# Kernel optimization log

Hardware: AMD Instinct MI355X
Metric: run time of the kernel (lower is better)

Reference implementation:

```python
import jax, jax.numpy as jnp
import numpy as np

PART = 0  # index of '<PART>' tag in vocab (select_part_tag = zeros)
W = 3     # max_word_len


def lstm_scan(x_seq, h0, c0, Wih, Whh, bih, bhh):
    """x_seq: [S, N, D] -> outputs [S, N, H]. torch LSTM gate order i, f, g, o."""
    def cell(carry, x):
        h, c = carry
        g = x @ Wih.T + bih + h @ Whh.T + bhh
        i, f, gg, o = jnp.split(g, 4, axis=-1)
        c = jax.nn.sigmoid(f) * c + jax.nn.sigmoid(i) * jnp.tanh(gg)
        h = jax.nn.sigmoid(o) * jnp.tanh(c)
        return (h, c), h
    _, hs = jax.lax.scan(cell, (h0, c0), x_seq)
    return hs


def decoder_probs(win, h0, emb, Wih, Whh, bih, bhh, Wp, bp):
    """Decoder.forward for all start positions at once.
    win: [N, W] candidate-word tokens; h0: [N, H] (used as both h0 and c0).
    Returns [W, N]: row y = log p(word win[:, :y+1] then <PART>)."""
    N = win.shape[0]
    toks = jnp.concatenate([jnp.full((N, 1), PART, win.dtype), win], axis=1)  # prepend <PART>
    x = jnp.swapaxes(emb[toks], 0, 1)                    # [W+1, N, D]
    hs = lstm_scan(x, h0, h0, Wih, Whh, bih, bhh)        # [W+1, N, H]
    logits = hs @ Wp.T + bp                              # [W+1, N, V]
    logZ = jax.nn.logsumexp(logits, axis=-1)             # [W+1, N]
    # log_softmax gathered at target char / <PART> tag positions
    char = jnp.take_along_axis(logits[:-1], win.T[:, :, None], axis=-1)[..., 0] - logZ[:-1]  # [W, N]
    tag = logits[1:, :, PART] - logZ[1:]                 # [W, N]
    return jnp.cumsum(char, axis=0) + tag                # cumulative char logprob + end tag


def forward_loss(sentence, emb, enc, decf, decb):
    B, T = sentence.shape
    H = enc[1].shape[1]
    fvec = sentence
    bvec = jnp.flip(sentence, axis=1)

    def encode(vec):
        toks = jnp.concatenate([jnp.full((B, 1), PART, vec.dtype), vec[:, :-1]], axis=1)
        x = jnp.swapaxes(emb[toks], 0, 1)                # [T, B, D]
        z = jnp.zeros((B, H), emb.dtype)
        return lstm_scan(x, z, z, *enc)                  # [T, B, H]

    enc_f, enc_b = encode(fvec), encode(bvec)
    idx = jnp.clip(jnp.arange(T)[:, None] + jnp.arange(W)[None, :], 0, T - 1)  # [T, W]

    def run_dec(vec, enc_out, params):
        win = vec[:, idx].reshape(B * T, W)              # window starting at each position
        h0 = jnp.swapaxes(enc_out, 0, 1).reshape(B * T, -1)
        p = decoder_probs(win, h0, emb, *params)         # [W, B*T]
        return p.reshape(W, B, T).transpose(2, 0, 1)     # [T(start), W(len-1), B]

    fwdP = run_dec(fvec, enc_f, decf)
    bwdP = run_dec(bvec, enc_b, decb)

    xs = jnp.arange(T)[:, None]
    ys = jnp.arange(W)[None, :]
    # SGB_A.add_bidirection: P[x, y, b] = score of word of length y+1 ending at position x
    P = 0.5 * (fwdP[jnp.clip(xs - ys, 0, T - 1), ys] + bwdP[T - 1 - xs, ys])  # [T, W, B]

    # compute_all_probability: semi-CRF forward recursion
    NEG = jnp.asarray(-1e30, P.dtype)
    def step(buf, inp):
        # buf[i] = total[j-1-i]
        p_j, j = inp
        cand = jnp.where((jnp.arange(W) < j)[:, None], buf + p_j, NEG)
        tot = jax.nn.logsumexp(cand, axis=0)
        return jnp.concatenate([tot[None], buf[:-1]], axis=0), tot

    _, totals = jax.lax.scan(step, jnp.zeros((W, B), P.dtype), (P, jnp.arange(1, T + 1)))
    return -jnp.mean(totals[-1])


def setup_inputs() -> dict:
    key = jax.random.key(0)
    V, D, H, B, T = 8000, 256, 256, 16, 128
    ks = jax.random.split(key, 24)
    s_d = 1.0 / np.sqrt(D)
    s_h = 1.0 / np.sqrt(H)

    def mat(k, shape, scale):
        return jax.random.normal(k, shape, jnp.float32) * scale

    def lstm_p(k):
        k1, k2, k3, k4 = jax.random.split(k, 4)
        return (mat(k1, (4 * H, D), s_d), mat(k2, (4 * H, H), s_h),
                mat(k3, (4 * H,), s_h), mat(k4, (4 * H,), s_h))

    enc = lstm_p(ks[1])
    decf_l = lstm_p(ks[2])
    decb_l = lstm_p(ks[3])
    inp = {
        "sentence": jax.random.randint(ks[0], (B, T), 0, V, jnp.int32),
        "emb": mat(ks[4], (V, D), 1.0),
        "enc_Wih": enc[0], "enc_Whh": enc[1], "enc_bih": enc[2], "enc_bhh": enc[3],
        "decf_Wih": decf_l[0], "decf_Whh": decf_l[1], "decf_bih": decf_l[2], "decf_bhh": decf_l[3],
        "decf_Wp": mat(ks[5], (V, H), s_h), "decf_bp": mat(ks[6], (V,), s_h),
        "decb_Wih": decb_l[0], "decb_Whh": decb_l[1], "decb_bih": decb_l[2], "decb_bhh": decb_l[3],
        "decb_Wp": mat(ks[7], (V, H), s_h), "decb_bp": mat(ks[8], (V,), s_h),
    }
    return inp


def reference(sentence, emb, enc_Wih, enc_Whh, enc_bih, enc_bhh,
              decf_Wih, decf_Whh, decf_bih, decf_bhh, decf_Wp, decf_bp,
              decb_Wih, decb_Whh, decb_bih, decb_bhh, decb_Wp, decb_bp):
    return forward_loss(
        sentence, emb,
        (enc_Wih, enc_Whh, enc_bih, enc_bhh),
        (decf_Wih, decf_Whh, decf_bih, decf_bhh, decf_Wp, decf_bp),
        (decb_Wih, decb_Whh, decb_bih, decb_bhh, decb_Wp, decb_bp))
```

## Files before the change

kernel.cpp:

```cpp
#include <hip/hip_runtime.h>
#include <math.h>

#define VOCAB 8000
#define NN 2048

typedef unsigned short u16;
typedef __attribute__((ext_vector_type(8))) short short8v;
typedef __attribute__((ext_vector_type(4))) short short4v;
typedef __attribute__((ext_vector_type(4))) float float4v;
typedef __attribute__((ext_vector_type(4))) int int4v;

#define OFF_WPBF   0ul
#define OFF_WDEC   2048000ul
#define OFF_XENC   2572288ul
#define OFF_H0BF   4153344ul
#define OFF_DECX   4677632ul
#define OFF_CDEC   6250496ul
#define OFF_HSBF   7299072ul
#define OFF_GBUF   9396224ul
#define OFF_LOGZ   13590528ul
#define OFF_GCH    13606912ul
#define OFF_GTG    13619200ul
#define OFF_P      13631488ul
#define OFF_WTOK   13637632ul
#define OFF_XP0    13649920ul
#define OFF_ENCW   13652032ul
#define OFF_SENC   13914240ul
#define OFF_SQ     13915264ul
#define OFF_WQI8   13916288ul
#define OFF_GXD    13981824ul
#define WS_NEED_OV ((OFF_GXD + 6291456ul) * 4ul)

__device__ __forceinline__ float sigf(float x) { return 1.0f / (1.0f + __expf(-x)); }
__device__ __forceinline__ float tanhsafe(float x) {
    x = fminf(15.0f, fmaxf(-15.0f, x));
    float e = __expf(2.0f * x);
    return (e - 1.0f) / (e + 1.0f);
}
__device__ __forceinline__ u16 f2bf(float f) {
    union { float f; unsigned int u; } x; x.f = f;
    return (u16)((x.u + 0x7fffu + ((x.u >> 16) & 1u)) >> 16);
}
__device__ __forceinline__ float bf2f(u16 x) {
    union { unsigned int u; float f; } v; v.u = ((unsigned int)x) << 16;
    return v.f;
}

__device__ __forceinline__ short8v ldfrag(const u16* lds, int row, int k, int lane, int SB) {
    int r = row + (lane & 15);
    int off = r * SB + ((k + ((lane >> 4) << 3)) << 1);
    off ^= (r & 7) << 4;
    return *(const short8v*)((const char*)lds + off);
}

__device__ __forceinline__ void stage128x256(const u16* __restrict__ g, int row0, int rowmax,
                                             int rowstride, int col0, u16* lds, int tid) {
    #pragma unroll
    for (int it = 0; it < 16; ++it) {
        int chunk = tid + it * 256;
        int r = chunk >> 5;
        int kc = (chunk & 31) << 3;
        short8v v = {0, 0, 0, 0, 0, 0, 0, 0};
        if (row0 + r < rowmax)
            v = *(const short8v*)(g + (size_t)(row0 + r) * rowstride + col0 + kc);
        int off = (r * 512 + kc * 2) ^ ((r & 7) << 4);
        *(short8v*)((char*)lds + off) = v;
    }
}

__global__ __launch_bounds__(256) void k_setup(const int* __restrict__ S,
                                               const float* __restrict__ emb,
                                               const float* __restrict__ eWih, const float* __restrict__ eWhh,
                                               const float* __restrict__ fWih, const float* __restrict__ fWhh,
                                               const float* __restrict__ fWp,
                                               const float* __restrict__ bWih, const float* __restrict__ bWhh,
                                               const float* __restrict__ bWp,
                                               u16* __restrict__ WpBF, u16* __restrict__ WdecBF,
                                               u16* __restrict__ encW,
                                               float* __restrict__ s_enc, signed char* __restrict__ wq,
                                               u16* __restrict__ xEncBF,
                                               u16* __restrict__ decX, int* __restrict__ winTok,
                                               float* __restrict__ xp0) {
    const int b = blockIdx.x, tid = threadIdx.x;
    if (b < 2000) {
        int chunk = b * 256 + tid;
        int kc = (chunk & 31) << 3;
        int v = (chunk >> 5) % 8000;
        int d = chunk / (8000 * 32);
        const float* src = (d ? bWp : fWp) + (size_t)v * 256 + kc;
        u16 t8[8];
        #pragma unroll
        for (int j = 0; j < 8; ++j) t8[j] = f2bf(src[j]);
        *(short8v*)(WpBF + ((size_t)d * 8000 + v) * 256 + kc) = *(short8v*)t8;
    } else if (b < 2512) {
        int chunk = (b - 2000) * 256 + tid;
        int kc = (chunk & 63) << 3;
        int r = (chunk >> 6) & 1023;
        int d = chunk >> 16;
        const float* Whh = d ? bWhh : fWhh;
        const float* Wih = d ? bWih : fWih;
        const float* src = (kc < 256) ? (Whh + (size_t)r * 256 + kc) : (Wih + (size_t)r * 256 + (kc - 256));
        u16 t8[8];
        #pragma unroll
        for (int j = 0; j < 8; ++j) t8[j] = f2bf(src[j]);
        *(short8v*)(WdecBF + ((size_t)d * 1024 + r) * 512 + kc) = *(short8v*)t8;
    } else if (b < 2768) {
        int chunk = (b - 2512) * 256 + tid;
        int kc = (chunk & 63) << 3;
        int r = chunk >> 6;
        const float* src = (kc < 256) ? (eWhh + (size_t)r * 256 + kc) : (eWih + (size_t)r * 256 + (kc - 256));
        u16 t8[8];
        #pragma unroll
        for (int j = 0; j < 8; ++j) t8[j] = f2bf(src[j]);
        *(short8v*)(encW + (size_t)r * 512 + kc) = *(short8v*)t8;
    } else if (b < 2832) {
        int lin = (b - 2768) * 256 + tid;
        int lane = lin & 63;
        int ks = (lin >> 6) & 3;
        int c = (lin >> 8) & 3;
        int w = lin >> 10;
        int r = c * 256 + w * 16 + (lane & 15);
        float m = 0.0f;
        for (int k = 0; k < 256; k += 4) {
            float4 v4 = *(const float4*)(eWhh + (size_t)r * 256 + k);
            m = fmaxf(m, fmaxf(fmaxf(fabsf(v4.x), fabsf(v4.y)), fmaxf(fabsf(v4.z), fabsf(v4.w))));
        }
        float sqv = (m > 0.0f) ? 127.0f / m : 0.0f;
        if (ks == 0 && lane < 16) s_enc[r] = m / 16129.0f;
        int kb = ks * 64 + ((lane >> 4) << 4);
        signed char o16[16];
        #pragma unroll
        for (int j = 0; j < 16; ++j) {
            float q = rintf(eWhh[(size_t)r * 256 + kb + j] * sqv);
            q = fminf(127.0f, fmaxf(-127.0f, q));
            o16[j] = (signed char)q;
        }
        *(int4v*)(wq + (size_t)lin * 16) = *(int4v*)o16;
    } else if (b < 3344) {
        int chunk = (b - 2832) * 256 + tid;
        int kc = (chunk & 31) << 3;
        int bb = (chunk >> 5) & 15;
        int t = (chunk >> 9) & 127;
        int d = chunk >> 16;
        int tok = 0;
        if (t > 0) tok = d ? S[bb * 128 + 128 - t] : S[bb * 128 + t - 1];
        const float* src = emb + (size_t)tok * 256 + kc;
        u16 t8[8];
        #pragma unroll
        for (int j = 0; j < 8; ++j) t8[j] = f2bf(src[j]);
        *(short8v*)(xEncBF + (size_t)(((d * 128 + t) * 16) + bb) * 256 + kc) = *(short8v*)t8;
    } else if (b < 4880) {
        int chunk = (b - 3344) * 256 + tid;
        int kc = (chunk & 31) << 3;
        int n = (chunk >> 5) & 2047;
        int r2 = chunk >> 16;
        int s = r2 % 3, d = r2 / 3;
        int bb = n >> 7, tq = n & 127;
        int pos = min(tq + s, 127);
        int tok = d ? S[bb * 128 + 127 - pos] : S[bb * 128 + pos];
        const float* src = emb + (size_t)tok * 256 + kc;
        u16 t8[8];
        #pragma unroll
        for (int j = 0; j < 8; ++j) t8[j] = f2bf(src[j]);
        *(short8v*)(decX + ((size_t)(d * 3 + s) * NN + n) * 256 + kc) = *(short8v*)t8;
        if ((chunk & 31) == 0) winTok[(d * 3 + s) * NN + n] = tok;
    } else {
        int idx = (b - 4880) * 256 + tid;
        int d = idx >> 10, r = idx & 1023;
        const float* Wih = d ? bWih : fWih;
        float acc = 0.0f;
        for (int k = 0; k < 256; ++k) acc = fmaf(emb[k], Wih[r * 256 + k], acc);
        xp0[idx] = acc;
    }
}

__global__ __launch_bounds__(256) void k_xproj(const u16* __restrict__ xEncBF,
                                               const u16* __restrict__ encW,
                                               const float* __restrict__ ebih,
                                               const float* __restrict__ ebhh,
                                               float* __restrict__ xpT) {
    __shared__ u16 At[128 * 256];
    __shared__ u16 Bt[128 * 256];
    const int tid = threadIdx.x, lane = tid & 63, wid = tid >> 6;
    const int wm = wid >> 1, wv = wid & 1;
    const int r0 = blockIdx.x * 128, n0 = blockIdx.y * 128, d = blockIdx.z;
    stage128x256(xEncBF + (size_t)d * 2048 * 256, n0, 1 << 30, 256, 0, At, tid);
    stage128x256(encW, r0, 1 << 30, 512, 256, Bt, tid);
    __syncthreads();
    float4v acc[4][4];
    #pragma unroll
    for (int m = 0; m < 4; ++m)
        #pragma unroll
        for (int v = 0; v < 4; ++v) acc[m][v] = (float4v){0.f, 0.f, 0.f, 0.f};
    #pragma unroll
    for (int k = 0; k < 8; ++k) {
        short8v af[4], bf[4];
        #pragma unroll
        for (int m = 0; m < 4; ++m) af[m] = ldfrag(At, wm * 64 + m * 16, k * 32, lane, 512);
        #pragma unroll
        for (int v = 0; v < 4; ++v) bf[v] = ldfrag(Bt, wv * 64 + v * 16, k * 32, lane, 512);
        #pragma unroll
        for (int m = 0; m < 4; ++m)
            #pragma unroll
            for (int v = 0; v < 4; ++v)
                acc[m][v] = __builtin_amdgcn_mfma_f32_16x16x32_bf16(af[m], bf[v], acc[m][v], 0, 0, 0);
    }
    float bs[4]; int rg[4];
    #pragma unroll
    for (int v = 0; v < 4; ++v) {
        rg[v] = r0 + wv * 64 + v * 16 + (lane & 15);
        bs[v] = ebih[rg[v]] + ebhh[rg[v]];
    }
    #pragma unroll
    for (int m = 0; m < 4; ++m)
        #pragma unroll
        for (int i = 0; i < 4; ++i) {
            int n = n0 + wm * 64 + m * 16 + ((lane >> 4) << 2) + i;
            int t_ = n >> 4, bfull = n & 15;
            #pragma unroll
            for (int v = 0; v < 4; ++v) {
                int g = rg[v] >> 8, u = rg[v] & 255;
                size_t idx4 = (((size_t)(d * 16 + bfull) * 128 + t_) * 16 + (u >> 4)) * 16 + (u & 15);
                xpT[idx4 * 4 + g] = acc[m][v][i] + bs[v];
            }
        }
}

__global__ __launch_bounds__(1024) void k_encx(const signed char* __restrict__ wq,
                                               const float* __restrict__ s_enc,
                                               const float4v* __restrict__ xpT4,
                                               u16* __restrict__ h0bf,
                                               const u16* __restrict__ decXBF,
                                               const u16* __restrict__ WdecBF,
                                               const float* __restrict__ fbih, const float* __restrict__ fbhh,
                                               const float* __restrict__ bbih, const float* __restrict__ bbhh,
                                               u16* __restrict__ gXdec) {
    __shared__ char smem[131072];
    const int tid = threadIdx.x, lane = tid & 63, w = tid >> 6;
    const int l15 = lane & 15, hi = lane >> 4;
    if (blockIdx.x < 32) {
        signed char (*hbuf)[4096] = (signed char(*)[4096])smem;
        const int blk = blockIdx.x, d = blk >> 4, b = blk & 15;
        int4v breg[4][4];
        #pragma unroll
        for (int c = 0; c < 4; ++c)
            #pragma unroll
            for (int ks = 0; ks < 4; ++ks)
                breg[c][ks] = *(const int4v*)(wq + ((size_t)(((w * 4 + c) * 4 + ks) * 64 + lane)) * 16);
        float sreg[4];
        #pragma unroll
        for (int c = 0; c < 4; ++c) sreg[c] = s_enc[c * 256 + w * 16 + l15];
        float creg = 0.0f;
        ((long*)hbuf)[tid & 1023] = 0l;
        const bool cellane = (lane < 16);
        const int u = w * 16 + l15;
        const float4v* xbase = xpT4 + ((size_t)(d * 16 + b) * 128) * 256 + w * 16 + l15;
        float4v xv_next = {0.f, 0.f, 0.f, 0.f};
        if (cellane) xv_next = xbase[0];
        __syncthreads();
        for (int t = 0; t < 128; ++t) {
            int cur = t & 1;
            float4v xv = xv_next;
            if (cellane && t < 127) xv_next = xbase[(size_t)(t + 1) * 256];
            int4v af[4];
            #pragma unroll
            for (int ks = 0; ks < 4; ++ks) {
                int off = (l15 * 256 + ks * 64 + hi * 16) ^ ((l15 & 7) << 4);
                af[ks] = *(const int4v*)(hbuf[cur] + off);
            }
            int4v acc[4];
            #pragma unroll
            for (int c = 0; c < 4; ++c) {
                acc[c] = (int4v){0, 0, 0, 0};
                #pragma unroll
                for (int ks = 0; ks < 4; ++ks)
                    acc[c] = __builtin_amdgcn_mfma_i32_16x16x64_i8(af[ks], breg[c][ks], acc[c], 0, 0, 0);
            }
            if (cellane) {
                float gi = (float)acc[0][0] * sreg[0] + xv[0];
                float gf = (float)acc[1][0] * sreg[1] + xv[1];
                float gG = (float)acc[2][0] * sreg[2] + xv[2];
                float go = (float)acc[3][0] * sreg[3] + xv[3];
                float cn = sigf(gf) * creg + sigf(gi) * tanhsafe(gG);
                float h = sigf(go) * tanhsafe(cn);
                creg = cn;
                h0bf[((size_t)d * NN + b * 128 + t) * 256 + u] = f2bf(h);
                hbuf[cur ^ 1][u] = (signed char)rintf(h * 127.0f);
            }
            __syncthreads();
        }
    } else {
        u16* At = (u16*)smem;
        u16* Bt = (u16*)(smem + 65536);
        const int bi = blockIdx.x - 32;
        const int rt = bi & 7, nt = (bi >> 3) & 15, rest = bi >> 7;
        const int sx = rest % 3, d = rest / 3;
        const int r0 = rt * 128, n0 = nt * 128;
        const int wm = w >> 2, wv = w & 3;
        const u16* Asrc = decXBF + (size_t)(d * 3 + sx) * NN * 256;
        const u16* Bsrc = WdecBF + (size_t)d * 1024 * 512;
        #pragma unroll
        for (int it = 0; it < 4; ++it) {
            int chunk = tid + it * 1024;
            int r = chunk >> 5, kc = (chunk & 31) << 3;
            short8v va = *(const short8v*)(Asrc + (size_t)(n0 + r) * 256 + kc);
            short8v vb = *(const short8v*)(Bsrc + (size_t)(r0 + r) * 512 + 256 + kc);
            int off = (r * 512 + kc * 2) ^ ((r & 7) << 4);
            *(short8v*)((char*)At + off) = va;
            *(short8v*)((char*)Bt + off) = vb;
        }
        __syncthreads();
        float4v acc[2][2];
        #pragma unroll
        for (int m = 0; m < 2; ++m)
            #pragma unroll
            for (int v = 0; v < 2; ++v) acc[m][v] = (float4v){0.f, 0.f, 0.f, 0.f};
        #pragma unroll
        for (int kk = 0; kk < 8; ++kk) {
            short8v af[2], bf[2];
            #pragma unroll
            for (int m = 0; m < 2; ++m) af[m] = ldfrag(At, wm * 32 + m * 16, kk * 32, lane, 512);
            #pragma unroll
            for (int v = 0; v < 2; ++v) bf[v] = ldfrag(Bt, wv * 32 + v * 16, kk * 32, lane, 512);
            #pragma unroll
            for (int m = 0; m < 2; ++m)
                #pragma unroll
                for (int v = 0; v < 2; ++v)
                    acc[m][v] = __builtin_amdgcn_mfma_f32_16x16x32_bf16(af[m], bf[v], acc[m][v], 0, 0, 0);
        }
        const float* bih = d ? bbih : fbih;
        const float* bhh = d ? bbhh : fbhh;
        #pragma unroll
        for (int m = 0; m < 2; ++m)
            #pragma unroll
            for (int i = 0; i < 4; ++i) {
                int n = n0 + wm * 32 + m * 16 + hi * 4 + i;
                #pragma unroll
                for (int v = 0; v < 2; ++v) {
                    int r = r0 + wv * 32 + v * 16 + l15;
                    float val = acc[m][v][i] + bih[r] + bhh[r];
                    gXdec[((size_t)(d * 3 + sx) * NN + n) * 1024 + r] = f2bf(val);
                }
            }
    }
}

__global__ __launch_bounds__(256) void k_decmm(const u16* __restrict__ Ah, size_t ahStride,
                                               const u16* __restrict__ Axx, size_t axStride,
                                               const u16* __restrict__ Wdec,
                                               const float* __restrict__ bihf, const float* __restrict__ bhhf,
                                               const float* __restrict__ bihb, const float* __restrict__ bhhb,
                                               const float* __restrict__ xp0, int s,
                                               const u16* __restrict__ gXdec,
                                               float* __restrict__ gBuf) {
    __shared__ u16 At[128 * 256];
    __shared__ u16 Bt[128 * 256];
    const int tid = threadIdx.x, lane = tid & 63, wid = tid >> 6;
    const int wm = wid >> 1, wv = wid & 1;
    const int r0 = blockIdx.x * 128, n0 = blockIdx.y * 128, d = blockIdx.z;
    float4v acc[4][4];
    #pragma unroll
    for (int m = 0; m < 4; ++m)
        #pragma unroll
        for (int v = 0; v < 4; ++v) acc[m][v] = (float4v){0.f, 0.f, 0.f, 0.f};
    const int useX = (s >= 1);
    const int nph = (useX && !gXdec) ? 2 : 1;
    for (int ph = 0; ph < nph; ++ph) {
        const u16* Asrc = (ph == 0) ? (Ah + (size_t)d * ahStride) : (Axx + (size_t)d * axStride);
        stage128x256(Asrc, n0, 1 << 30, 256, 0, At, tid);
        stage128x256(Wdec + (size_t)d * 1024 * 512, r0, 1 << 30, 512, ph * 256, Bt, tid);
        __syncthreads();
        #pragma unroll
        for (int k = 0; k < 8; ++k) {
            short8v af[4], bf[4];
            #pragma unroll
            for (int m = 0; m < 4; ++m) af[m] = ldfrag(At, wm * 64 + m * 16, k * 32, lane, 512);
            #pragma unroll
            for (int v = 0; v < 4; ++v) bf[v] = ldfrag(Bt, wv * 64 + v * 16, k * 32, lane, 512);
            #pragma unroll
            for (int m = 0; m < 4; ++m)
                #pragma unroll
                for (int v = 0; v < 4; ++v)
                    acc[m][v] = __builtin_amdgcn_mfma_f32_16x16x32_bf16(af[m], bf[v], acc[m][v], 0, 0, 0);
        }
        __syncthreads();
    }
    const float* bih = d ? bihb : bihf;
    const float* bhh = d ? bhhb : bhhf;
    int rg[4];
    float bs[4] = {0.f, 0.f, 0.f, 0.f};
    #pragma unroll
    for (int v = 0; v < 4; ++v) {
        rg[v] = r0 + wv * 64 + v * 16 + (lane & 15);
        if (!useX) bs[v] = bih[rg[v]] + bhh[rg[v]] + xp0[d * 1024 + rg[v]];
        else if (!gXdec) bs[v] = bih[rg[v]] + bhh[rg[v]];
    }
    #pragma unroll
    for (int m = 0; m < 4; ++m)
        #pragma unroll
        for (int i = 0; i < 4; ++i) {
            int n = n0 + wm * 64 + m * 16 + ((lane >> 4) << 2) + i;
            #pragma unroll
            for (int v = 0; v < 4; ++v) {
                float g = acc[m][v][i] + bs[v];
                if (useX && gXdec)
                    g += bf2f(gXdec[((size_t)(d * 3 + s - 1) * NN + n) * 1024 + rg[v]]);
                gBuf[((size_t)d * NN + n) * 1024 + rg[v]] = g;
            }
        }
}

__global__ __launch_bounds__(256) void k_deccell(const float* __restrict__ gBuf,
                                                 const u16* __restrict__ h0bf,
                                                 float* __restrict__ cDec,
                                                 u16* __restrict__ hsBF, int s) {
    int flat = blockIdx.x * 256 + threadIdx.x;
    int j = flat & 255;
    int n = (flat >> 8) & 2047;
    int d = flat >> 19;
    const float* g = gBuf + ((size_t)d * NN + n) * 1024;
    float gi = g[j], gf = g[j + 256], gg = g[j + 512], go = g[j + 768];
    float cprev = (s == 0) ? bf2f(h0bf[flat]) : cDec[flat];
    float cn = sigf(gf) * cprev + sigf(gi) * tanhsafe(gg);
    float h = sigf(go) * tanhsafe(cn);
    cDec[flat] = cn;
    hsBF[((size_t)(d * 4 + s) * NN + n) * 256 + j] = f2bf(h);
}

__global__ __launch_bounds__(512, 2) void k_proj8(const u16* __restrict__ hsBF,
                                                  const u16* __restrict__ WpBF,
                                                  const float* __restrict__ bpf, const float* __restrict__ bpb,
                                                  const int* __restrict__ winTok,
                                                  float* __restrict__ partials,
                                                  float* __restrict__ gchar, float* __restrict__ gtag) {
    __shared__ u16 At[128 * 256];
    __shared__ u16 Bt[2][64 * 256];
    const int tid = threadIdx.x, lane = tid & 63, w = tid >> 6;
    const int wm = w >> 1, wv = w & 1;
    const int l15 = lane & 15, hi = lane >> 4;
    const int L = blockIdx.x;
    const int chunkI = L & 7, idx = L >> 3;
    const int n0 = (idx & 15) * 128, d = idx >> 4;
    const int vt0 = chunkI * 16;
    const int nvt = min(16, 125 - vt0);
    const float* bp = d ? bpb : bpf;

#define LOADB8(vt_) do {                                                          \
        _Pragma("unroll")                                                         \
        for (int it = 0; it < 4; ++it) {                                          \
            int g = tid + it * 512; int r = g >> 5, kc = (g & 31) << 3;           \
            bregs[it] = *(const short8v*)(WpBF + ((size_t)d * 8000 + (vt_) * 64 + r) * 256 + kc); \
        }                                                                         \
    } while (0)
#define WRITEB8(buf_) do {                                                        \
        _Pragma("unroll")                                                         \
        for (int it = 0; it < 4; ++it) {                                          \
            int g = tid + it * 512; int r = g >> 5, kc = (g & 31) << 3;           \
            int off = (r * 512 + kc * 2) ^ ((r & 7) << 4);                        \
            *(short8v*)((char*)Bt[buf_] + off) = bregs[it];                       \
        }                                                                         \
    } while (0)

    short8v bregs[4];
    for (int s = 0; s < 4; ++s) {
        const u16* hsA = hsBF + (size_t)(d * 4 + s) * NN * 256;
        #pragma unroll
        for (int it = 0; it < 8; ++it) {
            int chunk = tid + it * 512;
            int r = chunk >> 5, kc = (chunk & 31) << 3;
            short8v v8 = *(const short8v*)(hsA + (size_t)(n0 + r) * 256 + kc);
            int off = (r * 512 + kc * 2) ^ ((r & 7) << 4);
            *(short8v*)((char*)At + off) = v8;
        }
        LOADB8(vt0);
        WRITEB8(0);
        int tok[2][4];
        #pragma unroll
        for (int m = 0; m < 2; ++m)
            #pragma unroll
            for (int i = 0; i < 4; ++i) {
                int n = n0 + wm * 32 + m * 16 + hi * 4 + i;
                tok[m][i] = (s < 3) ? winTok[(d * 3 + s) * NN + n] : -1;
            }
        float expsum[2][4] = {{0.f, 0.f, 0.f, 0.f}, {0.f, 0.f, 0.f, 0.f}};
        __syncthreads();
        short8v afr[2][8];
        #pragma unroll
        for (int m = 0; m < 2; ++m)
            #pragma unroll
            for (int kk = 0; kk < 8; ++kk) {
                afr[m][kk] = ldfrag(At, wm * 32 + m * 16, kk * 32, lane, 512);
                asm volatile("" : "+v"(afr[m][kk]));
            }
        int cur = 0;
        for (int t = 0; t < nvt; ++t) {
            int vt = vt0 + t;
            if (t + 1 < nvt) LOADB8(vt + 1);
            float bpv[2];
            #pragma unroll
            for (int v = 0; v < 2; ++v) bpv[v] = bp[vt * 64 + wv * 32 + v * 16 + l15];
            float4v acc[2][2];
            #pragma unroll
            for (int m = 0; m < 2; ++m)
                #pragma unroll
                for (int v = 0; v < 2; ++v) acc[m][v] = (float4v){0.f, 0.f, 0.f, 0.f};
            #pragma unroll
            for (int kk = 0; kk < 8; ++kk) {
                short8v bf[2];
                #pragma unroll
                for (int v = 0; v < 2; ++v) bf[v] = ldfrag(Bt[cur], wv * 32 + v * 16, kk * 32, lane, 512);
                #pragma unroll
                for (int m = 0; m < 2; ++m)
                    #pragma unroll
                    for (int v = 0; v < 2; ++v)
                        acc[m][v] = __builtin_amdgcn_mfma_f32_16x16x32_bf16(afr[m][kk], bf[v], acc[m][v], 0, 0, 0);
            }
            #pragma unroll
            for (int m = 0; m < 2; ++m)
                #pragma unroll
                for (int i = 0; i < 4; ++i) {
                    int n = n0 + wm * 32 + m * 16 + hi * 4 + i;
                    float es = 0.0f;
                    #pragma unroll
                    for (int v = 0; v < 2; ++v) {
                        int vgv = vt * 64 + wv * 32 + v * 16 + l15;
                        float lg = acc[m][v][i] + bpv[v];
                        es += __expf(lg);
                        if (vgv == tok[m][i]) gchar[(d * 3 + s) * NN + n] = lg;
                        if (s >= 1 && vgv == 0) gtag[(d * 3 + (s - 1)) * NN + n] = lg;
                    }
                    expsum[m][i] += es;
                }
            __syncthreads();
            if (t + 1 < nvt) WRITEB8(cur ^ 1);
            __syncthreads();
            cur ^= 1;
        }
        #pragma unroll
        for (int m = 0; m < 2; ++m)
            #pragma unroll
            for (int i = 0; i < 4; ++i) {
                float e = expsum[m][i];
                #pragma unroll
                for (int off = 1; off <= 8; off <<= 1) e += __shfl_xor(e, off);
                if (l15 == 0) {
                    int n = n0 + wm * 32 + m * 16 + hi * 4 + i;
                    partials[((size_t)(d * 4 + s) * NN + n) * 16 + chunkI * 2 + wv] = e;
                }
            }
    }
#undef LOADB8
#undef WRITEB8
}

__global__ __launch_bounds__(256) void k_lzsum(const float* __restrict__ partials,
                                               float* __restrict__ logZ) {
    int row = blockIdx.x * 256 + threadIdx.x;
    const float* p = partials + (size_t)row * 16;
    float s = 0.0f;
    #pragma unroll
    for (int c = 0; c < 16; ++c) s += p[c];
    logZ[row] = __logf(s);
}

__global__ __launch_bounds__(256) void k_passm(const float* __restrict__ gchar,
                                               const float* __restrict__ gtag,
                                               const float* __restrict__ logZ,
                                               float* __restrict__ P) {
    int flat = blockIdx.x * 256 + threadIdx.x;
    if (flat >= 128 * 3 * 16) return;
    int b = flat & 15;
    int y = (flat >> 4) % 3;
    int x = flat / 48;
    int nf = b * 128 + min(127, max(0, x - y));
    int nb = b * 128 + 127 - x;
    float pf = 0.0f, pb = 0.0f;
    for (int ss = 0; ss <= y; ++ss) {
        pf += gchar[ss * NN + nf] - logZ[ss * NN + nf];
        pb += gchar[(3 + ss) * NN + nb] - logZ[(4 + ss) * NN + nb];
    }
    pf += gtag[y * NN + nf] - logZ[(y + 1) * NN + nf];
    pb += gtag[(3 + y) * NN + nb] - logZ[(4 + y + 1) * NN + nb];
    P[flat] = 0.5f * (pf + pb);
}

__global__ __launch_bounds__(64) void k_scan(const float* __restrict__ P, float* __restrict__ out) {
    __shared__ float Pl[128 * 48];
    int tid = threadIdx.x;
    #pragma unroll
    for (int it = 0; it < 96; ++it) Pl[tid + it * 64] = P[tid + it * 64];
    __syncthreads();
    if (tid < 16) {
        int b = tid;
        float b0 = 0.f, b1 = 0.f, b2 = 0.f, tot = 0.f;
        for (int j = 1; j <= 128; ++j) {
            float c0 = b0 + Pl[((j - 1) * 3 + 0) * 16 + b];
            float c1 = (j >= 2) ? b1 + Pl[((j - 1) * 3 + 1) * 16 + b] : -1e30f;
            float c2 = (j >= 3) ? b2 + Pl[((j - 1) * 3 + 2) * 16 + b] : -1e30f;
            float mx = fmaxf(c0, fmaxf(c1, c2));
            float sv = __expf(c0 - mx) + __expf(c1 - mx) + __expf(c2 - mx);
            tot = mx + __logf(sv);
            b2 = b1; b1 = b0; b0 = tot;
        }
        #pragma unroll
        for (int off = 1; off <= 8; off <<= 1) tot += __shfl_xor(tot, off);
        if (b == 0) out[0] = -tot / 16.0f;
    }
}

extern "C" void kernel_launch(void* const* d_in, const int* in_sizes, int n_in,
                              void* d_out, int out_size, void* d_ws, size_t ws_size,
                              hipStream_t stream) {
    const int* S = (const int*)d_in[0];
    const float* emb = (const float*)d_in[1];
    const float* eWih = (const float*)d_in[2];
    const float* eWhh = (const float*)d_in[3];
    const float* ebih = (const float*)d_in[4];
    const float* ebhh = (const float*)d_in[5];
    const float* fWih = (const float*)d_in[6];
    const float* fWhh = (const float*)d_in[7];
    const float* fbih = (const float*)d_in[8];
    const float* fbhh = (const float*)d_in[9];
    const float* fWp  = (const float*)d_in[10];
    const float* fbp  = (const float*)d_in[11];
    const float* bWih = (const float*)d_in[12];
    const float* bWhh = (const float*)d_in[13];
    const float* bbih = (const float*)d_in[14];
    const float* bbhh = (const float*)d_in[15];
    const float* bWp  = (const float*)d_in[16];
    const float* bbp  = (const float*)d_in[17];

    float* w = (float*)d_ws;
    u16* WpBF    = (u16*)(w + OFF_WPBF);
    u16* WdecBF  = (u16*)(w + OFF_WDEC);
    u16* xEncBF  = (u16*)(w + OFF_XENC);
    u16* h0bf    = (u16*)(w + OFF_H0BF);
    u16* decXBF  = (u16*)(w + OFF_DECX);
    float* cDec  = w + OFF_CDEC;
    u16* hsBF    = (u16*)(w + OFF_HSBF);
    float* gBuf  = w + OFF_GBUF;
    float* xpT   = gBuf;
    float* partials = gBuf;
    float* logZ  = w + OFF_LOGZ;
    float* gchar = w + OFF_GCH;
    float* gtag  = w + OFF_GTG;
    float* Pm    = w + OFF_P;
    int* winTok  = (int*)(w + OFF_WTOK);
    float* xp0   = w + OFF_XP0;
    u16* encW    = (u16*)(w + OFF_ENCW);
    float* sEnc  = w + OFF_SENC;
    signed char* wqEnc = (signed char*)(w + OFF_WQI8);
    u16* gXdec   = (u16*)(w + OFF_GXD);

    const bool useOv = (ws_size >= WS_NEED_OV);

    k_setup<<<4888, 256, 0, stream>>>(S, emb, eWih, eWhh, fWih, fWhh, fWp,
                                      bWih, bWhh, bWp,
                                      WpBF, WdecBF, encW, sEnc, wqEnc,
                                      xEncBF, decXBF, winTok, xp0);

    k_xproj<<<dim3(8, 16, 2), 256, 0, stream>>>(xEncBF, encW, ebih, ebhh, xpT);

    k_encx<<<useOv ? 800 : 32, 1024, 0, stream>>>(wqEnc, sEnc, (const float4v*)xpT, h0bf,
                                                  decXBF, WdecBF, fbih, fbhh, bbih, bbhh,
                                                  gXdec);

    const u16* gx = useOv ? gXdec : nullptr;
    for (int s = 0; s < 4; ++s) {
        const u16* Ah; size_t ahS;
        const u16* Axx; size_t axS;
        if (s == 0) {
            Ah = h0bf; ahS = (size_t)NN * 256;
            Axx = decXBF; axS = (size_t)3 * NN * 256;
        } else {
            Ah = hsBF + (size_t)(s - 1) * NN * 256; ahS = (size_t)4 * NN * 256;
            Axx = decXBF + (size_t)(s - 1) * NN * 256; axS = (size_t)3 * NN * 256;
        }
        k_decmm<<<dim3(8, 16, 2), 256, 0, stream>>>(Ah, ahS, Axx, axS, WdecBF,
                                                    fbih, fbhh, bbih, bbhh, xp0,
                                                    s, gx, gBuf);
        k_deccell<<<4096, 256, 0, stream>>>(gBuf, h0bf, cDec, hsBF, s);
    }

    k_proj8<<<256, 512, 0, stream>>>(hsBF, WpBF, fbp, bbp, winTok,
                                     partials, gchar, gtag);
    k_lzsum<<<64, 256, 0, stream>>>(partials, logZ);
    k_passm<<<24, 256, 0, stream>>>(gchar, gtag, logZ, Pm);
    k_scan<<<1, 64, 0, stream>>>(Pm, (float*)d_out);
}
```

Baseline: 473.3 us.

## Fuse decoder gate GEMM with LSTM cell and buffer encoder outputs in LDS

The decoder step's gate matmul and its LSTM cell update now run in one kernel. Each block stages the 32 hidden units' i/f/g/o weight rows, so all four gates for a unit sit in one tile. Gates go to shared memory and the cell runs in place, which drops the fp32 gBuf round trip through global memory and one launch per step. In the encoder, per-step h stores to global are replaced by an LDS history buffer copied out once at the end, and the x prefetch becomes a plain per-step load. The cost is 128KB of LDS per decoder block, which limits occupancy, and exposed x-load latency in the encoder.

```diff
diff --git a/kernel.cpp b/kernel.cpp
--- a/kernel.cpp
+++ b/kernel.cpp
@@ -240,6 +240,7 @@
     const int l15 = lane & 15, hi = lane >> 4;
     if (blockIdx.x < 32) {
         signed char (*hbuf)[4096] = (signed char(*)[4096])smem;
+        u16* hist = (u16*)(smem + 8192);
         const int blk = blockIdx.x, d = blk >> 4, b = blk & 15;
         int4v breg[4][4];
         #pragma unroll
@@ -255,13 +256,11 @@
         const bool cellane = (lane < 16);
         const int u = w * 16 + l15;
         const float4v* xbase = xpT4 + ((size_t)(d * 16 + b) * 128) * 256 + w * 16 + l15;
-        float4v xv_next = {0.f, 0.f, 0.f, 0.f};
-        if (cellane) xv_next = xbase[0];
         __syncthreads();
         for (int t = 0; t < 128; ++t) {
             int cur = t & 1;
-            float4v xv = xv_next;
-            if (cellane && t < 127) xv_next = xbase[(size_t)(t + 1) * 256];
+            float4v xv = {0.f, 0.f, 0.f, 0.f};
+            if (cellane) xv = xbase[(size_t)t * 256];
             int4v af[4];
             #pragma unroll
             for (int ks = 0; ks < 4; ++ks) {
@@ -284,11 +283,15 @@
                 float cn = sigf(gf) * creg + sigf(gi) * tanhsafe(gG);
                 float h = sigf(go) * tanhsafe(cn);
                 creg = cn;
-                h0bf[((size_t)d * NN + b * 128 + t) * 256 + u] = f2bf(h);
+                hist[t * 256 + u] = f2bf(h);
                 hbuf[cur ^ 1][u] = (signed char)rintf(h * 127.0f);
             }
             __syncthreads();
         }
+        long* dst = (long*)(h0bf + (size_t)(d * NN + b * 128) * 256);
+        const long* src = (const long*)hist;
+        #pragma unroll
+        for (int it = 0; it < 8; ++it) dst[tid + it * 1024] = src[tid + it * 1024];
     } else {
         u16* At = (u16*)smem;
         u16* Bt = (u16*)(smem + 65536);
@@ -345,19 +348,23 @@
     }
 }
 
-__global__ __launch_bounds__(256) void k_decmm(const u16* __restrict__ Ah, size_t ahStride,
-                                               const u16* __restrict__ Axx, size_t axStride,
-                                               const u16* __restrict__ Wdec,
-                                               const float* __restrict__ bihf, const float* __restrict__ bhhf,
-                                               const float* __restrict__ bihb, const float* __restrict__ bhhb,
-                                               const float* __restrict__ xp0, int s,
-                                               const u16* __restrict__ gXdec,
-                                               float* __restrict__ gBuf) {
-    __shared__ u16 At[128 * 256];
-    __shared__ u16 Bt[128 * 256];
+__global__ __launch_bounds__(256) void k_decf(const u16* __restrict__ Ah, size_t ahStride,
+                                              const u16* __restrict__ Axx, size_t axStride,
+                                              const u16* __restrict__ Wdec,
+                                              const float* __restrict__ bihf, const float* __restrict__ bhhf,
+                                              const float* __restrict__ bihb, const float* __restrict__ bhhb,
+                                              const float* __restrict__ xp0, int s,
+                                              const u16* __restrict__ gXdec,
+                                              const u16* __restrict__ h0bf,
+                                              float* __restrict__ cDec, u16* __restrict__ hsBF) {
+    __shared__ char smem[131072];
+    u16* At = (u16*)smem;
+    u16* Bt = (u16*)(smem + 65536);
+    float* gl = (float*)smem;
     const int tid = threadIdx.x, lane = tid & 63, wid = tid >> 6;
     const int wm = wid >> 1, wv = wid & 1;
-    const int r0 = blockIdx.x * 128, n0 = blockIdx.y * 128, d = blockIdx.z;
+    const int l15 = lane & 15, hi = lane >> 4;
+    const int u0 = blockIdx.x * 32, n0 = blockIdx.y * 128, d = blockIdx.z;
     float4v acc[4][4];
     #pragma unroll
     for (int m = 0; m < 4; ++m)
@@ -368,7 +375,15 @@
     for (int ph = 0; ph < nph; ++ph) {
         const u16* Asrc = (ph == 0) ? (Ah + (size_t)d * ahStride) : (Axx + (size_t)d * axStride);
         stage128x256(Asrc, n0, 1 << 30, 256, 0, At, tid);
-        stage128x256(Wdec + (size_t)d * 1024 * 512, r0, 1 << 30, 512, ph * 256, Bt, tid);
+        #pragma unroll
+        for (int it = 0; it < 16; ++it) {
+            int chunk = tid + it * 256;
+            int rl = chunk >> 5, kc = (chunk & 31) << 3;
+            int rglob = ((rl >> 5) << 8) + u0 + (rl & 31);
+            short8v v8 = *(const short8v*)(Wdec + ((size_t)d * 1024 + rglob) * 512 + ph * 256 + kc);
+            int off = (rl * 512 + kc * 2) ^ ((rl & 7) << 4);
+            *(short8v*)((char*)Bt + off) = v8;
+        }
         __syncthreads();
         #pragma unroll
         for (int k = 0; k < 8; ++k) {
@@ -387,44 +402,39 @@
     }
     const float* bih = d ? bihb : bihf;
     const float* bhh = d ? bhhb : bhhf;
-    int rg[4];
-    float bs[4] = {0.f, 0.f, 0.f, 0.f};
-    #pragma unroll
-    for (int v = 0; v < 4; ++v) {
-        rg[v] = r0 + wv * 64 + v * 16 + (lane & 15);
-        if (!useX) bs[v] = bih[rg[v]] + bhh[rg[v]] + xp0[d * 1024 + rg[v]];
-        else if (!gXdec) bs[v] = bih[rg[v]] + bhh[rg[v]];
-    }
     #pragma unroll
     for (int m = 0; m < 4; ++m)
         #pragma unroll
         for (int i = 0; i < 4; ++i) {
-            int n = n0 + wm * 64 + m * 16 + ((lane >> 4) << 2) + i;
+            int nl = wm * 64 + m * 16 + hi * 4 + i;
             #pragma unroll
             for (int v = 0; v < 4; ++v) {
-                float g = acc[m][v][i] + bs[v];
-                if (useX && gXdec)
-                    g += bf2f(gXdec[((size_t)(d * 3 + s - 1) * NN + n) * 1024 + rg[v]]);
-                gBuf[((size_t)d * NN + n) * 1024 + rg[v]] = g;
-            }
-        }
-}
-
-__global__ __launch_bounds__(256) void k_deccell(const float* __restrict__ gBuf,
-                                                 const u16* __restrict__ h0bf,
-                                                 float* __restrict__ cDec,
-                                                 u16* __restrict__ hsBF, int s) {
-    int flat = blockIdx.x * 256 + threadIdx.x;
-    int j = flat & 255;
-    int n = (flat >> 8) & 2047;
-    int d = flat >> 19;
-    const float* g = gBuf + ((size_t)d * NN + n) * 1024;
-    float gi = g[j], gf = g[j + 256], gg = g[j + 512], go = g[j + 768];
-    float cprev = (s == 0) ? bf2f(h0bf[flat]) : cDec[flat];
-    float cn = sigf(gf) * cprev + sigf(gi) * tanhsafe(gg);
-    float h = sigf(go) * tanhsafe(cn);
-    cDec[flat] = cn;
-    hsBF[((size_t)(d * 4 + s) * NN + n) * 256 + j] = f2bf(h);
+                int rl = wv * 64 + v * 16 + l15;
+                int rglob = ((rl >> 5) << 8) + u0 + (rl & 31);
+                float g = acc[m][v][i];
+                if (!useX) g += bih[rglob] + bhh[rglob] + xp0[d * 1024 + rglob];
+                else if (gXdec) g += bf2f(gXdec[((size_t)(d * 3 + s - 1) * NN + n0 + nl) * 1024 + rglob]);
+                else g += bih[rglob] + bhh[rglob];
+                gl[nl * 128 + rl] = g;
+            }
+        }
+    __syncthreads();
+    #pragma unroll
+    for (int it = 0; it < 16; ++it) {
+        int item = tid + it * 256;
+        int ul = item & 31, nl = item >> 5;
+        float gi = gl[nl * 128 + ul];
+        float gf = gl[nl * 128 + 32 + ul];
+        float gg = gl[nl * 128 + 64 + ul];
+        float go = gl[nl * 128 + 96 + ul];
+        int j = u0 + ul, n = n0 + nl;
+        size_t flat = ((size_t)d * NN + n) * 256 + j;
+        float cprev = (s == 0) ? bf2f(h0bf[flat]) : cDec[flat];
+        float cn = sigf(gf) * cprev + sigf(gi) * tanhsafe(gg);
+        float h = sigf(go) * tanhsafe(cn);
+        cDec[flat] = cn;
+        hsBF[((size_t)(d * 4 + s) * NN + n) * 256 + j] = f2bf(h);
+    }
 }
 
 __global__ __launch_bounds__(512, 2) void k_proj8(const u16* __restrict__ hsBF,
@@ -676,10 +686,9 @@
             Ah = hsBF + (size_t)(s - 1) * NN * 256; ahS = (size_t)4 * NN * 256;
             Axx = decXBF + (size_t)(s - 1) * NN * 256; axS = (size_t)3 * NN * 256;
         }
-        k_decmm<<<dim3(8, 16, 2), 256, 0, stream>>>(Ah, ahS, Axx, axS, WdecBF,
-                                                    fbih, fbhh, bbih, bbhh, xp0,
-                                                    s, gx, gBuf);
-        k_deccell<<<4096, 256, 0, stream>>>(gBuf, h0bf, cDec, hsBF, s);
+        k_decf<<<dim3(8, 16, 2), 256, 0, stream>>>(Ah, ahS, Axx, axS, WdecBF,
+                                                   fbih, fbhh, bbih, bbhh, xp0,
+                                                   s, gx, h0bf, cDec, hsBF);
     }
 
     k_proj8<<<256, 512, 0, stream>>>(hsBF, WpBF, fbp, bbp, winTok,
```

After: 482.6 us. About the same (+2.0%).
